# Optimization experiments

Measured on AMD Instinct MI355X. Metric: run time of the kernel, lower is better.

## Reference

```python
import jax, jax.numpy as jnp
import numpy as np
import math

L, E, H, T, B, V = 6, 768, 12, 1024, 4, 256
HS = E // H


def _ln(x, w, b, eps=1e-5):
    mu = jnp.mean(x, axis=-1, keepdims=True)
    var = jnp.mean((x - mu) ** 2, axis=-1, keepdims=True)
    return (x - mu) * jax.lax.rsqrt(var + eps) * w + b


def setup_inputs() -> dict:
    key = jax.random.key(0)
    ks = jax.random.split(key, 12)
    std = 0.02
    inp = {
        "idx": jax.random.randint(ks[0], (B, T), 0, V, dtype=jnp.int64),
        "tok_emb": jax.random.normal(ks[1], (V, E), jnp.float32) * std,
        "pos_emb": jnp.zeros((1, T, E), jnp.float32),
        "ln1_w": jnp.ones((L, E), jnp.float32),
        "ln1_b": jnp.zeros((L, E), jnp.float32),
        "Wq": jax.random.normal(ks[2], (L, E, E), jnp.float32) * std,
        "bq": jnp.zeros((L, E), jnp.float32),
        "Wk": jax.random.normal(ks[3], (L, E, E), jnp.float32) * std,
        "bk": jnp.zeros((L, E), jnp.float32),
        "Wv": jax.random.normal(ks[4], (L, E, E), jnp.float32) * std,
        "bv": jnp.zeros((L, E), jnp.float32),
        "Wp": jax.random.normal(ks[5], (L, E, E), jnp.float32) * std,
        "bp": jnp.zeros((L, E), jnp.float32),
        "ln2_w": jnp.ones((L, E), jnp.float32),
        "ln2_b": jnp.zeros((L, E), jnp.float32),
        "W1": jax.random.normal(ks[6], (L, E, 4 * E), jnp.float32) * std,
        "b1": jnp.zeros((L, 4 * E), jnp.float32),
        "W2": jax.random.normal(ks[7], (L, 4 * E, E), jnp.float32) * std,
        "b2": jnp.zeros((L, E), jnp.float32),
        "lnf_w": jnp.ones((E,), jnp.float32),
        "lnf_b": jnp.zeros((E,), jnp.float32),
        "lm_head": jax.random.normal(ks[8], (E, V), jnp.float32) * std,
    }
    return inp


def reference(idx, tok_emb, pos_emb, ln1_w, ln1_b, Wq, bq, Wk, bk, Wv, bv, Wp, bp,
              ln2_w, ln2_b, W1, b1, W2, b2, lnf_w, lnf_b, lm_head):
    Bc, Tc = idx.shape
    causal = jnp.tril(jnp.ones((Tc, Tc), bool))  # [T,T]
    scale = 1.0 / math.sqrt(HS)
    x = tok_emb[idx] + pos_emb[:, :Tc, :]  # [B,T,E]
    for l in range(L):
        h = _ln(x, ln1_w[l], ln1_b[l])
        q = (h @ Wq[l] + bq[l]).reshape(Bc, Tc, H, HS).transpose(0, 2, 1, 3)
        k = (h @ Wk[l] + bk[l]).reshape(Bc, Tc, H, HS).transpose(0, 2, 1, 3)
        v = (h @ Wv[l] + bv[l]).reshape(Bc, Tc, H, HS).transpose(0, 2, 1, 3)
        att = jnp.einsum('bhtd,bhsd->bhts', q, k) * scale  # [B,H,T,T]
        att = jnp.where(causal, att, -jnp.inf)
        att = jax.nn.softmax(att, axis=-1)
        y = jnp.einsum('bhts,bhsd->bhtd', att, v)
        y = y.transpose(0, 2, 1, 3).reshape(Bc, Tc, E)
        x = x + (y @ Wp[l] + bp[l])
        h2 = _ln(x, ln2_w[l], ln2_b[l])
        m = jax.nn.gelu(h2 @ W1[l] + b1[l], approximate=False)
        x = x + (m @ W2[l] + b2[l])
    x = _ln(x, lnf_w, lnf_b)
    logits = x @ lm_head  # [B,T,V]
    return logits
```

## Files before the change

kernel.cpp:

```cpp
#include <hip/hip_runtime.h>

#define L_ 6
#define E_ 768
#define H_ 12
#define T_ 1024
#define B_ 4
#define V_ 256
#define M_ (B_*T_)
#define E4_ (4*E_)
#define QKVN (3*E_)
#define NZ_ 4

typedef __bf16 bf16;
typedef __bf16 bf16x8 __attribute__((ext_vector_type(8)));
typedef __bf16 bf16x4 __attribute__((ext_vector_type(4)));
typedef float f32x4 __attribute__((ext_vector_type(4)));

#define GF_GELU     1
#define GF_BIAS_EXT 16
#define GF_PART     32

__device__ __forceinline__ float ldf(const void* p, size_t i, int f32m) {
    return f32m ? ((const float*)p)[i] : (float)((const bf16*)p)[i];
}

__device__ __forceinline__ void async_cp16(const void* g, void* l) {
    __builtin_amdgcn_global_load_lds(
        (__attribute__((address_space(1))) void*)g,
        (__attribute__((address_space(3))) void*)l, 16, 0, 0);
}

__device__ __forceinline__ float exp2_hw(float x) {
    float r; asm("v_exp_f32 %0, %1" : "=v"(r) : "v"(x)); return r;
}

__global__ __launch_bounds__(256) void k_probe(const void* __restrict__ tok,
    const void* __restrict__ idxp, int* __restrict__ dm)
{
    __shared__ int sc1, sc2;
    if (threadIdx.x == 0) { sc1 = 0; sc2 = 0; }
    __syncthreads();
    const bf16* tb = (const bf16*)tok;
    int c1 = 0;
    for (int i = threadIdx.x; i < 4096; i += 256) {
        float v = (float)tb[2 * i];
        if (!(fabsf(v) < 100.f)) c1++;
    }
    const int* ip = (const int*)idxp;
    int c2 = 0;
    for (int i = threadIdx.x; i < 1024; i += 256)
        if (ip[2 * i + 1] != 0) c2++;
    atomicAdd(&sc1, c1);
    atomicAdd(&sc2, c2);
    __syncthreads();
    if (threadIdx.x == 0) { dm[0] = (sc1 > 400) ? 1 : 0; dm[1] = (sc2 < 100) ? 1 : 0; }
}

__global__ __launch_bounds__(256) void k_embed(const void* __restrict__ idxp,
    const void* __restrict__ tok, const void* __restrict__ pos,
    float* __restrict__ x, const int* __restrict__ dm)
{
    int f32m = dm[0], i64m = dm[1];
    int bt = blockIdx.x;
    int t  = bt & (T_ - 1);
    int id = i64m ? ((const int*)idxp)[2 * bt] : ((const int*)idxp)[bt];
    float* xo = x + (size_t)bt * E_;
    for (int e = threadIdx.x; e < E_; e += 256)
        xo[e] = ldf(tok, (size_t)id * E_ + e, f32m) + ldf(pos, (size_t)t * E_ + e, f32m);
}

__global__ __launch_bounds__(256) void k_ln(const float* __restrict__ x,
    const void* __restrict__ w, const void* __restrict__ b, size_t wboff,
    bf16* __restrict__ out, const int* __restrict__ dm)
{
    int f32m = dm[0];
    int row = blockIdx.x;
    int tid = threadIdx.x;
    const float* xr = x + (size_t)row * E_;
    float v0 = xr[tid], v1 = xr[tid + 256], v2 = xr[tid + 512];
    float s  = v0 + v1 + v2;
    float s2 = v0*v0 + v1*v1 + v2*v2;
    for (int off = 32; off; off >>= 1) {
        s  += __shfl_xor(s,  off);
        s2 += __shfl_xor(s2, off);
    }
    __shared__ float ls[4], ls2[4];
    int wave = tid >> 6;
    if ((tid & 63) == 0) { ls[wave] = s; ls2[wave] = s2; }
    __syncthreads();
    s  = ls[0] + ls[1] + ls[2] + ls[3];
    s2 = ls2[0] + ls2[1] + ls2[2] + ls2[3];
    float mu  = s * (1.0f / E_);
    float var = s2 * (1.0f / E_) - mu * mu;
    float rs  = rsqrtf(var + 1e-5f);
    bf16* o = out + (size_t)row * E_;
    o[tid]       = (bf16)(((v0 - mu) * rs) * ldf(w, wboff + tid,       f32m) + ldf(b, wboff + tid,       f32m));
    o[tid + 256] = (bf16)(((v1 - mu) * rs) * ldf(w, wboff + tid + 256, f32m) + ldf(b, wboff + tid + 256, f32m));
    o[tid + 512] = (bf16)(((v2 - mu) * rs) * ldf(w, wboff + tid + 512, f32m) + ldf(b, wboff + tid + 512, f32m));
}

__global__ __launch_bounds__(256) void k_red_ln(float* __restrict__ x,
    const float* __restrict__ part,
    const void* __restrict__ gb, size_t gboff,
    const void* __restrict__ w, const void* __restrict__ b, size_t wboff,
    bf16* __restrict__ out, const int* __restrict__ dm)
{
    const size_t PSTR = (size_t)M_ * E_;
    int f32m = dm[0];
    int row = blockIdx.x;
    int tid = threadIdx.x;
    float* xr = x + (size_t)row * E_;
    const float* pr = part + (size_t)row * E_;
    float v[3];
    #pragma unroll
    for (int j = 0; j < 3; j++) {
        int c = tid + j * 256;
        float acc = xr[c];
        #pragma unroll
        for (int z = 0; z < NZ_; z++) acc += pr[(size_t)z * PSTR + c];
        acc += ldf(gb, gboff + c, f32m);
        v[j] = acc;
        xr[c] = acc;
    }
    float s  = v[0] + v[1] + v[2];
    float s2 = v[0]*v[0] + v[1]*v[1] + v[2]*v[2];
    for (int off = 32; off; off >>= 1) {
        s  += __shfl_xor(s,  off);
        s2 += __shfl_xor(s2, off);
    }
    __shared__ float ls[4], ls2[4];
    int wave = tid >> 6;
    if ((tid & 63) == 0) { ls[wave] = s; ls2[wave] = s2; }
    __syncthreads();
    s  = ls[0] + ls[1] + ls[2] + ls[3];
    s2 = ls2[0] + ls2[1] + ls2[2] + ls2[3];
    float mu  = s * (1.0f / E_);
    float var = s2 * (1.0f / E_) - mu * mu;
    float rs  = rsqrtf(var + 1e-5f);
    bf16* o = out + (size_t)row * E_;
    #pragma unroll
    for (int j = 0; j < 3; j++) {
        int c = tid + j * 256;
        o[c] = (bf16)(((v[j] - mu) * rs) * ldf(w, wboff + c, f32m) + ldf(b, wboff + c, f32m));
    }
}

__global__ __launch_bounds__(256) void k_transpose(const void* __restrict__ in, size_t inoff,
    bf16* __restrict__ out, int R, int C, const int* __restrict__ dm)
{
    int f32m = dm[0];
    __shared__ bf16 tile[32][33];
    int r0 = blockIdx.x * 32, c0 = blockIdx.y * 32;
    int tx = threadIdx.x & 31, ty = threadIdx.x >> 5;
    #pragma unroll
    for (int i = 0; i < 4; i++)
        tile[ty + 8*i][tx] = (bf16)ldf(in, inoff + (size_t)(r0 + ty + 8*i) * C + (c0 + tx), f32m);
    __syncthreads();
    #pragma unroll
    for (int i = 0; i < 4; i++)
        out[(size_t)(c0 + ty + 8*i) * R + (r0 + tx)] = tile[tx][ty + 8*i];
}

__global__ __launch_bounds__(256) void k_transpose3(const void* __restrict__ a,
    const void* __restrict__ b, const void* __restrict__ c, size_t inoff,
    bf16* __restrict__ out, int R, int C, const int* __restrict__ dm)
{
    int f32m = dm[0];
    const void* in = (blockIdx.z == 0) ? a : ((blockIdx.z == 1) ? b : c);
    bf16* o = out + (size_t)blockIdx.z * R * C;
    __shared__ bf16 tile[32][33];
    int r0 = blockIdx.x * 32, c0 = blockIdx.y * 32;
    int tx = threadIdx.x & 31, ty = threadIdx.x >> 5;
    #pragma unroll
    for (int i = 0; i < 4; i++)
        tile[ty + 8*i][tx] = (bf16)ldf(in, inoff + (size_t)(r0 + ty + 8*i) * C + (c0 + tx), f32m);
    __syncthreads();
    #pragma unroll
    for (int i = 0; i < 4; i++)
        o[(size_t)(c0 + ty + 8*i) * R + (r0 + tx)] = tile[tx][ty + 8*i];
}

__global__ __launch_bounds__(256) void k_cat3(const void* __restrict__ a,
    const void* __restrict__ b, const void* __restrict__ c, size_t voff,
    bf16* __restrict__ o, const int* __restrict__ dm)
{
    int f32m = dm[0];
    int i = blockIdx.x * 256 + threadIdx.x;
    float v = (i < E_) ? ldf(a, voff + i, f32m)
            : ((i < 2*E_) ? ldf(b, voff + i - E_, f32m) : ldf(c, voff + i - 2*E_, f32m));
    o[i] = (bf16)v;
}

__global__ __launch_bounds__(256) void k_cast_red(const float* __restrict__ in,
    void* __restrict__ out, const int* __restrict__ dm)
{
    const size_t S = (size_t)M_ * V_ / 4;
    size_t i = (size_t)blockIdx.x * 256 + threadIdx.x;
    const f32x4* p = (const f32x4*)in;
    f32x4 v = p[i];
    v += p[S + i];
    v += p[2*S + i];
    v += p[3*S + i];
    if (dm[0]) {
        ((f32x4*)out)[i] = v;
    } else {
        bf16x4 o;
        #pragma unroll
        for (int j = 0; j < 4; j++) o[j] = (bf16)v[j];
        ((bf16x4*)out)[i] = o;
    }
}

__global__ __launch_bounds__(256) void k_gemm(const bf16* __restrict__ A,
    const bf16* __restrict__ BT, const void* __restrict__ bias, size_t boff,
    void* __restrict__ outp, int M, int N, int K, int flags, const int* __restrict__ dm)
{
    int f32m = dm[0];
    __shared__ __attribute__((aligned(16))) bf16 As[128 * 64];
    __shared__ __attribute__((aligned(16))) bf16 Bs[128 * 64];
    int tid = threadIdx.x;
    int bn0 = blockIdx.x * 128, bm0 = blockIdx.y * 128;
    int kz = blockIdx.z;
    int Ks = K / gridDim.z;
    int kbeg = kz * Ks, kend = kbeg + Ks;
    int wave = tid >> 6, lane = tid & 63, quad = lane >> 4, l16 = lane & 15;
    int wr = wave >> 1, wc = wave & 1;

    int st_col = 8 * ((lane & 7) ^ (lane >> 3));
    int st_row_base = wave * 32 + (lane >> 3);

    f32x4 acc[4][4];
    #pragma unroll
    for (int i = 0; i < 4; i++)
        #pragma unroll
        for (int j = 0; j < 4; j++)
            acc[i][j] = (f32x4){0.f, 0.f, 0.f, 0.f};

    int sw = l16 & 7;
    for (int k0 = kbeg; k0 < kend; k0 += 64) {
        #pragma unroll
        for (int i = 0; i < 4; i++) {
            int row = st_row_base + i * 8;
            const bf16* ga = A  + (size_t)(bm0 + row) * K + k0 + st_col;
            const bf16* gb = BT + (size_t)(bn0 + row) * K + k0 + st_col;
            bf16* la = As + (size_t)(wave * 256 + i * 64) * 8;
            bf16* lb = Bs + (size_t)(wave * 256 + i * 64) * 8;
            async_cp16(ga, la);
            async_cp16(gb, lb);
        }
        __syncthreads();
        #pragma unroll
        for (int ks = 0; ks < 2; ks++) {
            bf16x8 af[4], bfr[4];
            #pragma unroll
            for (int mi = 0; mi < 4; mi++) {
                int row = wr*64 + mi*16 + l16;
                int kgs = (4*ks + quad) ^ sw;
                af[mi] = *(const bf16x8*)&As[row*64 + kgs*8];
            }
            #pragma unroll
            for (int ni = 0; ni < 4; ni++) {
                int row = wc*64 + ni*16 + l16;
                int kgs = (4*ks + quad) ^ sw;
                bfr[ni] = *(const bf16x8*)&Bs[row*64 + kgs*8];
            }
            #pragma unroll
            for (int mi = 0; mi < 4; mi++)
                #pragma unroll
                for (int ni = 0; ni < 4; ni++)
                    acc[mi][ni] = __builtin_amdgcn_mfma_f32_16x16x32_bf16(af[mi], bfr[ni], acc[mi][ni], 0, 0, 0);
        }
        __syncthreads();
    }

    float* pout = (float*)outp + (size_t)kz * M * N;
    #pragma unroll
    for (int mi = 0; mi < 4; mi++) {
        #pragma unroll
        for (int ni = 0; ni < 4; ni++) {
            int col = bn0 + wc*64 + ni*16 + l16;
            float bv = 0.f;
            if (bias)
                bv = (flags & GF_BIAS_EXT) ? ldf(bias, boff + col, f32m)
                                           : (float)((const bf16*)bias)[col];
            #pragma unroll
            for (int r = 0; r < 4; r++) {
                int row = bm0 + wr*64 + mi*16 + quad*4 + r;
                float val = acc[mi][ni][r] + bv;
                if (flags & GF_GELU) val = 0.5f * val * (1.f + erff(val * 0.70710678118f));
                size_t oidx = (size_t)row * N + col;
                if (flags & GF_PART) pout[oidx] = val;
                else                 ((bf16*)outp)[oidx] = (bf16)val;
            }
        }
    }
}

__device__ __forceinline__ void attn_qk_softmax(
    const bf16x8 qf[2], f32x4 OT[4], float& m_ln, float& l_ln,
    const bf16 (*Ks)[72], bf16 (*Ps)[72],
    int wave, int quad, int l16, int s0, int qt0, bool diag)
{
    f32x4 S[4];
    #pragma unroll
    for (int i = 0; i < 4; i++) S[i] = (f32x4){0.f, 0.f, 0.f, 0.f};
    #pragma unroll
    for (int ks = 0; ks < 2; ks++)
        #pragma unroll
        for (int ni = 0; ni < 4; ni++) {
            bf16x8 kf = *(const bf16x8*)&Ks[ni*16 + l16][ks*32 + quad*8];
            S[ni] = __builtin_amdgcn_mfma_f32_16x16x32_bf16(kf, qf[ks], S[ni], 0, 0, 0);
        }
    const float SC = 0.18033688011112042f;
    if (diag) {
        int qr = qt0 + wave*16 + l16;
        #pragma unroll
        for (int ni = 0; ni < 4; ni++)
            #pragma unroll
            for (int r = 0; r < 4; r++) {
                int scol = s0 + ni*16 + quad*4 + r;
                S[ni][r] = (scol > qr) ? -1e30f : S[ni][r] * SC;
            }
    } else {
        #pragma unroll
        for (int ni = 0; ni < 4; ni++)
            #pragma unroll
            for (int r = 0; r < 4; r++) S[ni][r] *= SC;
    }
    float tn[4];
    #pragma unroll
    for (int ni = 0; ni < 4; ni++)
        tn[ni] = fmaxf(fmaxf(S[ni][0], S[ni][1]), fmaxf(S[ni][2], S[ni][3]));
    float tm = fmaxf(fmaxf(tn[0], tn[1]), fmaxf(tn[2], tn[3]));
    tm = fmaxf(tm, __shfl_xor(tm, 16));
    tm = fmaxf(tm, __shfl_xor(tm, 32));
    float mnew = fmaxf(m_ln, tm);
    float alpha = exp2_hw(m_ln - mnew);
    m_ln = mnew;
    float rsum = 0.f;
    bf16x4 pk[4];
    #pragma unroll
    for (int ni = 0; ni < 4; ni++)
        #pragma unroll
        for (int r = 0; r < 4; r++) {
            float p = exp2_hw(S[ni][r] - mnew);
            rsum += p;
            pk[ni][r] = (bf16)p;
        }
    rsum += __shfl_xor(rsum, 16);
    rsum += __shfl_xor(rsum, 32);
    l_ln = l_ln * alpha + rsum;
    #pragma unroll
    for (int ni = 0; ni < 4; ni++)
        #pragma unroll
        for (int r = 0; r < 4; r++) OT[ni][r] *= alpha;
    #pragma unroll
    for (int ni = 0; ni < 4; ni++)
        *(bf16x4*)&Ps[wave*16 + l16][ni*16 + quad*4] = pk[ni];
}

__device__ __forceinline__ void attn_pv(
    f32x4 OT[4], const bf16 (*Ps)[72], const bf16 (*Vt)[72],
    int wave, int quad, int l16)
{
    #pragma unroll
    for (int ks = 0; ks < 2; ks++) {
        bf16x8 pf = *(const bf16x8*)&Ps[wave*16 + l16][ks*32 + quad*8];
        #pragma unroll
        for (int ni = 0; ni < 4; ni++) {
            bf16x8 vf = *(const bf16x8*)&Vt[ni*16 + l16][ks*32 + quad*8];
            OT[ni] = __builtin_amdgcn_mfma_f32_16x16x32_bf16(vf, pf, OT[ni], 0, 0, 0);
        }
    }
}

__global__ __launch_bounds__(256) void k_attn(const bf16* __restrict__ qkv, bf16* __restrict__ y)
{
    int xA = blockIdx.x;
    int xB = 15 - xA;
    int qtA = xA * 64, qtB = xB * 64;
    int h = blockIdx.y, b = blockIdx.z;
    int tid = threadIdx.x, wave = tid >> 6, lane = tid & 63, quad = lane >> 4, l16 = lane & 15;

    const bf16* qb = qkv + (size_t)b * T_ * QKVN + h * 64;
    const bf16* kb = qb + E_;
    const bf16* vb = qb + 2 * E_;

    __shared__ __attribute__((aligned(16))) bf16 Ks[64][72];
    __shared__ __attribute__((aligned(16))) bf16 Vt[64][72];
    __shared__ __attribute__((aligned(16))) bf16 U1[64][72];
    __shared__ __attribute__((aligned(16))) bf16 PsA[64][72];

    bf16x8 qfA[2], qfB[2];
    {
        int qrA = qtA + wave * 16 + l16;
        int qrB = qtB + wave * 16 + l16;
        #pragma unroll
        for (int ks = 0; ks < 2; ks++) {
            qfA[ks] = *(const bf16x8*)(qb + (size_t)qrA * QKVN + ks*32 + quad*8);
            qfB[ks] = *(const bf16x8*)(qb + (size_t)qrB * QKVN + ks*32 + quad*8);
        }
    }

    f32x4 OA[4], OB[4];
    #pragma unroll
    for (int i = 0; i < 4; i++) { OA[i] = (f32x4){0.f,0.f,0.f,0.f}; OB[i] = (f32x4){0.f,0.f,0.f,0.f}; }
    float mA = -3.0e38f, lA = 0.f;
    float mB = -3.0e38f, lB = 0.f;

    for (int st = 0; st <= xB; st++) {
        int s0 = st * 64;
        bool doA = (st <= xA);
        #pragma unroll
        for (int i = 0; i < 2; i++) {
            int li = i * 256 + tid;
            int row = li >> 3;
            int col = (li & 7) * 8;
            *(bf16x8*)&Ks[row][col] = *(const bf16x8*)(kb + (size_t)(s0 + row) * QKVN + col);
            *(bf16x8*)&U1[row][col] = *(const bf16x8*)(vb + (size_t)(s0 + row) * QKVN + col);
        }
        __syncthreads();
        {
            int d = tid & 63;
            #pragma unroll
            for (int ii = 0; ii < 2; ii++) {
                int sb = (tid >> 6) * 2 + ii;
                bf16x8 tv;
                #pragma unroll
                for (int j = 0; j < 8; j++) tv[j] = U1[sb*8 + j][d];
                *(bf16x8*)&Vt[d][sb*8] = tv;
            }
        }
        __syncthreads();
        attn_qk_softmax(qfB, OB, mB, lB, Ks, U1,  wave, quad, l16, s0, qtB, st == xB);
        if (doA)
            attn_qk_softmax(qfA, OA, mA, lA, Ks, PsA, wave, quad, l16, s0, qtA, st == xA);
        asm volatile("s_waitcnt lgkmcnt(0)" ::: "memory");
        attn_pv(OB, U1,  Vt, wave, quad, l16);
        if (doA) attn_pv(OA, PsA, Vt, wave, quad, l16);
        __syncthreads();
    }

    float invB = 1.f / lB, invA = 1.f / lA;
    int qrowB = qtB + wave*16 + l16;
    int qrowA = qtA + wave*16 + l16;
    #pragma unroll
    for (int ni = 0; ni < 4; ni++) {
        bf16x4 ovB, ovA;
        #pragma unroll
        for (int r = 0; r < 4; r++) {
            ovB[r] = (bf16)(OB[ni][r] * invB);
            ovA[r] = (bf16)(OA[ni][r] * invA);
        }
        *(bf16x4*)&y[(size_t)(b * T_ + qrowB) * E_ + h*64 + ni*16 + quad*4] = ovB;
        *(bf16x4*)&y[(size_t)(b * T_ + qrowA) * E_ + h*64 + ni*16 + quad*4] = ovA;
    }
}

extern "C" void kernel_launch(void* const* d_in, const int* in_sizes, int n_in,
                              void* d_out, int out_size, void* d_ws, size_t ws_size,
                              hipStream_t stream)
{
    const void* idx     = d_in[0];
    const void* tok_emb = d_in[1];
    const void* pos_emb = d_in[2];
    const void* ln1_w   = d_in[3];
    const void* ln1_b   = d_in[4];
    const void* Wq      = d_in[5];
    const void* bq      = d_in[6];
    const void* Wk      = d_in[7];
    const void* bk      = d_in[8];
    const void* Wv      = d_in[9];
    const void* bv      = d_in[10];
    const void* Wp      = d_in[11];
    const void* bp      = d_in[12];
    const void* ln2_w   = d_in[13];
    const void* ln2_b   = d_in[14];
    const void* W1      = d_in[15];
    const void* b1      = d_in[16];
    const void* W2      = d_in[17];
    const void* b2      = d_in[18];
    const void* lnf_w   = d_in[19];
    const void* lnf_b   = d_in[20];
    const void* lm_head = d_in[21];

    char* base = (char*)d_ws;
    size_t off = 0;
    auto nxt = [&](size_t bytes) -> void* {
        void* p = base + off;
        off += (bytes + 255) & ~(size_t)255;
        return p;
    };
    int*   dm   = (int*)  nxt(256);
    float* x    = (float*)nxt((size_t)M_ * E_ * 4);
    bf16*  h    = (bf16*) nxt((size_t)M_ * E_ * 2);
    bf16*  qkv  = (bf16*) nxt((size_t)M_ * QKVN * 2);
    bf16*  yb   = (bf16*) nxt((size_t)M_ * E_ * 2);
    bf16*  mbuf = (bf16*) nxt((size_t)M_ * E4_ * 2);
    bf16*  wt   = (bf16*) nxt((size_t)E4_ * E_ * 2);
    bf16*  bcat = (bf16*) nxt((size_t)QKVN * 2);
    float* part = (float*)nxt((size_t)NZ_ * M_ * E_ * 4);
    (void)ws_size; (void)in_sizes; (void)n_in; (void)out_size;

    k_probe<<<1, 256, 0, stream>>>(tok_emb, idx, dm);
    k_embed<<<M_, 256, 0, stream>>>(idx, tok_emb, pos_emb, x, dm);

    k_ln<<<M_, 256, 0, stream>>>(x, ln1_w, ln1_b, 0, h, dm);

    for (int l = 0; l < L_; l++) {
        size_t woE  = (size_t)l * E_ * E_;
        size_t voE  = (size_t)l * E_;
        size_t woW1 = (size_t)l * E_ * E4_;
        size_t voE4 = (size_t)l * E4_;

        k_transpose3<<<dim3(E_/32, E_/32, 3), 256, 0, stream>>>(Wq, Wk, Wv, woE, wt, E_, E_, dm);
        k_cat3<<<QKVN/256, 256, 0, stream>>>(bq, bk, bv, voE, bcat, dm);
        k_gemm<<<dim3(QKVN/128, M_/128), 256, 0, stream>>>(h, wt, bcat, 0, qkv, M_, QKVN, E_, 0, dm);

        k_attn<<<dim3(8, H_, B_), 256, 0, stream>>>(qkv, yb);

        k_transpose<<<dim3(E_/32, E_/32), 256, 0, stream>>>(Wp, woE, wt, E_, E_, dm);
        k_gemm<<<dim3(E_/128, M_/128, NZ_), 256, 0, stream>>>(yb, wt, nullptr, 0, part, M_, E_, E_, GF_PART, dm);
        k_red_ln<<<M_, 256, 0, stream>>>(x, part, bp, voE, ln2_w, ln2_b, voE, h, dm);

        k_transpose<<<dim3(E_/32, E4_/32), 256, 0, stream>>>(W1, woW1, wt, E_, E4_, dm);
        k_gemm<<<dim3(E4_/128, M_/128), 256, 0, stream>>>(h, wt, b1, voE4, mbuf, M_, E4_, E_, GF_GELU | GF_BIAS_EXT, dm);

        k_transpose<<<dim3(E4_/32, E_/32), 256, 0, stream>>>(W2, woW1, wt, E4_, E_, dm);
        k_gemm<<<dim3(E_/128, M_/128, NZ_), 256, 0, stream>>>(mbuf, wt, nullptr, 0, part, M_, E_, E4_, GF_PART, dm);
        if (l < L_ - 1)
            k_red_ln<<<M_, 256, 0, stream>>>(x, part, b2, voE, ln1_w, ln1_b, (size_t)(l+1) * E_, h, dm);
        else
            k_red_ln<<<M_, 256, 0, stream>>>(x, part, b2, voE, lnf_w, lnf_b, 0, h, dm);
    }

    k_transpose<<<dim3(E_/32, V_/32), 256, 0, stream>>>(lm_head, 0, wt, E_, V_, dm);
    k_gemm<<<dim3(V_/128, M_/128, NZ_), 256, 0, stream>>>(h, wt, nullptr, 0, part, M_, V_, E_, GF_PART, dm);
    k_cast_red<<<(M_*V_)/1024, 256, 0, stream>>>(part, d_out, dm);
}
```

Before: 1.523 ms.

## Restructure attention to one query tile per block with async swizzled K/V prefetch

```diff
diff --git a/kernel.cpp b/kernel.cpp
--- a/kernel.cpp
+++ b/kernel.cpp
@@ -296,9 +296,9 @@
     }
 }
 
-__device__ __forceinline__ void attn_qk_softmax(
+__device__ __forceinline__ void attn_qk_softmax2(
     const bf16x8 qf[2], f32x4 OT[4], float& m_ln, float& l_ln,
-    const bf16 (*Ks)[72], bf16 (*Ps)[72],
+    const bf16* __restrict__ Kbuf, bf16 (*Ps)[72],
     int wave, int quad, int l16, int s0, int qt0, bool diag)
 {
     f32x4 S[4];
@@ -308,7 +308,8 @@
     for (int ks = 0; ks < 2; ks++)
         #pragma unroll
         for (int ni = 0; ni < 4; ni++) {
-            bf16x8 kf = *(const bf16x8*)&Ks[ni*16 + l16][ks*32 + quad*8];
+            int kg = (ks*4 + quad) ^ (l16 & 7);
+            bf16x8 kf = *(const bf16x8*)&Kbuf[(ni*16 + l16)*64 + kg*8];
             S[ni] = __builtin_amdgcn_mfma_f32_16x16x32_bf16(kf, qf[ks], S[ni], 0, 0, 0);
         }
     const float SC = 0.18033688011112042f;
@@ -376,9 +377,8 @@
 
 __global__ __launch_bounds__(256) void k_attn(const bf16* __restrict__ qkv, bf16* __restrict__ y)
 {
-    int xA = blockIdx.x;
-    int xB = 15 - xA;
-    int qtA = xA * 64, qtB = xB * 64;
+    int x = blockIdx.x;
+    int qt = x * 64;
     int h = blockIdx.y, b = blockIdx.z;
     int tid = threadIdx.x, wave = tid >> 6, lane = tid & 63, quad = lane >> 4, l16 = lane & 15;
 
@@ -386,74 +386,75 @@
     const bf16* kb = qb + E_;
     const bf16* vb = qb + 2 * E_;
 
-    __shared__ __attribute__((aligned(16))) bf16 Ks[64][72];
+    __shared__ __attribute__((aligned(16))) bf16 Kbuf[64 * 64];
+    __shared__ __attribute__((aligned(16))) bf16 Vbuf[64 * 64];
     __shared__ __attribute__((aligned(16))) bf16 Vt[64][72];
-    __shared__ __attribute__((aligned(16))) bf16 U1[64][72];
-    __shared__ __attribute__((aligned(16))) bf16 PsA[64][72];
-
-    bf16x8 qfA[2], qfB[2];
+    __shared__ __attribute__((aligned(16))) bf16 Ps[64][72];
+
+    int srow = tid >> 3;
+    int scol = 8 * ((lane & 7) ^ (srow & 7));
+
+    bf16x8 qf[2];
     {
-        int qrA = qtA + wave * 16 + l16;
-        int qrB = qtB + wave * 16 + l16;
-        #pragma unroll
-        for (int ks = 0; ks < 2; ks++) {
-            qfA[ks] = *(const bf16x8*)(qb + (size_t)qrA * QKVN + ks*32 + quad*8);
-            qfB[ks] = *(const bf16x8*)(qb + (size_t)qrB * QKVN + ks*32 + quad*8);
-        }
-    }
-
-    f32x4 OA[4], OB[4];
-    #pragma unroll
-    for (int i = 0; i < 4; i++) { OA[i] = (f32x4){0.f,0.f,0.f,0.f}; OB[i] = (f32x4){0.f,0.f,0.f,0.f}; }
-    float mA = -3.0e38f, lA = 0.f;
-    float mB = -3.0e38f, lB = 0.f;
-
-    for (int st = 0; st <= xB; st++) {
+        int qr = qt + wave * 16 + l16;
+        #pragma unroll
+        for (int ks = 0; ks < 2; ks++)
+            qf[ks] = *(const bf16x8*)(qb + (size_t)qr * QKVN + ks*32 + quad*8);
+    }
+
+    f32x4 OT[4];
+    #pragma unroll
+    for (int i = 0; i < 4; i++) OT[i] = (f32x4){0.f,0.f,0.f,0.f};
+    float m_ln = -3.0e38f, l_ln = 0.f;
+
+    auto stage = [&](int s0) {
+        #pragma unroll
+        for (int i = 0; i < 2; i++) {
+            int row = i * 32 + srow;
+            const bf16* gk = kb + (size_t)(s0 + row) * QKVN + scol;
+            const bf16* gv = vb + (size_t)(s0 + row) * QKVN + scol;
+            bf16* lk = Kbuf + ((size_t)i * 32 + wave * 8) * 64;
+            bf16* lv = Vbuf + ((size_t)i * 32 + wave * 8) * 64;
+            async_cp16(gk, lk);
+            async_cp16(gv, lv);
+        }
+    };
+
+    stage(0);
+    asm volatile("s_waitcnt vmcnt(0)" ::: "memory");
+    __syncthreads();
+
+    for (int st = 0; st <= x; st++) {
         int s0 = st * 64;
-        bool doA = (st <= xA);
-        #pragma unroll
-        for (int i = 0; i < 2; i++) {
-            int li = i * 256 + tid;
-            int row = li >> 3;
-            int col = (li & 7) * 8;
-            *(bf16x8*)&Ks[row][col] = *(const bf16x8*)(kb + (size_t)(s0 + row) * QKVN + col);
-            *(bf16x8*)&U1[row][col] = *(const bf16x8*)(vb + (size_t)(s0 + row) * QKVN + col);
-        }
-        __syncthreads();
         {
-            int d = tid & 63;
+            int d = lane;
+            int dg = d >> 3, de = d & 7;
             #pragma unroll
             for (int ii = 0; ii < 2; ii++) {
-                int sb = (tid >> 6) * 2 + ii;
+                int sb = wave * 2 + ii;
                 bf16x8 tv;
                 #pragma unroll
-                for (int j = 0; j < 8; j++) tv[j] = U1[sb*8 + j][d];
-                *(bf16x8*)&Vt[d][sb*8] = tv;
+                for (int j = 0; j < 8; j++)
+                    tv[j] = Vbuf[(sb*8 + j) * 64 + ((dg ^ j) * 8) + de];
+                *(bf16x8*)&Vt[d][sb * 8] = tv;
             }
         }
+        attn_qk_softmax2(qf, OT, m_ln, l_ln, Kbuf, Ps, wave, quad, l16, s0, qt, st == x);
         __syncthreads();
-        attn_qk_softmax(qfB, OB, mB, lB, Ks, U1,  wave, quad, l16, s0, qtB, st == xB);
-        if (doA)
-            attn_qk_softmax(qfA, OA, mA, lA, Ks, PsA, wave, quad, l16, s0, qtA, st == xA);
-        asm volatile("s_waitcnt lgkmcnt(0)" ::: "memory");
-        attn_pv(OB, U1,  Vt, wave, quad, l16);
-        if (doA) attn_pv(OA, PsA, Vt, wave, quad, l16);
+        if (st < x) stage(s0 + 64);
+        attn_pv(OT, Ps, Vt, wave, quad, l16);
+        asm volatile("s_waitcnt vmcnt(0)" ::: "memory");
         __syncthreads();
     }
 
-    float invB = 1.f / lB, invA = 1.f / lA;
-    int qrowB = qtB + wave*16 + l16;
-    int qrowA = qtA + wave*16 + l16;
+    float inv = 1.f / l_ln;
+    int qrow = qt + wave * 16 + l16;
     #pragma unroll
     for (int ni = 0; ni < 4; ni++) {
-        bf16x4 ovB, ovA;
-        #pragma unroll
-        for (int r = 0; r < 4; r++) {
-            ovB[r] = (bf16)(OB[ni][r] * invB);
-            ovA[r] = (bf16)(OA[ni][r] * invA);
-        }
-        *(bf16x4*)&y[(size_t)(b * T_ + qrowB) * E_ + h*64 + ni*16 + quad*4] = ovB;
-        *(bf16x4*)&y[(size_t)(b * T_ + qrowA) * E_ + h*64 + ni*16 + quad*4] = ovA;
+        bf16x4 ov;
+        #pragma unroll
+        for (int r = 0; r < 4; r++) ov[r] = (bf16)(OT[ni][r] * inv);
+        *(bf16x4*)&y[(size_t)(b * T_ + qrow) * E_ + h*64 + ni*16 + quad*4] = ov;
     }
 }
 
@@ -517,7 +518,7 @@
         k_cat3<<<QKVN/256, 256, 0, stream>>>(bq, bk, bv, voE, bcat, dm);
         k_gemm<<<dim3(QKVN/128, M_/128), 256, 0, stream>>>(h, wt, bcat, 0, qkv, M_, QKVN, E_, 0, dm);
 
-        k_attn<<<dim3(8, H_, B_), 256, 0, stream>>>(qkv, yb);
+        k_attn<<<dim3(16, H_, B_), 256, 0, stream>>>(qkv, yb);
 
         k_transpose<<<dim3(E_/32, E_/32), 256, 0, stream>>>(Wp, woE, wt, E_, E_, dm);
         k_gemm<<<dim3(E_/128, M_/128, NZ_), 256, 0, stream>>>(yb, wt, nullptr, 0, part, M_, E_, E_, GF_PART, dm);
```

Result: faster. 1.463 ms (-3.9%).
